# Kernel tuning notes

Measured on AMD Instinct MI355X. Metric: run time of the kernel, lower is better.

Reference implementation:

```python
import jax, jax.numpy as jnp
import numpy as np

B, T, D, H, W = 2, 16, 64, 64, 64
K = 3      # kernel_size
EXP = 2    # mlp expand
EPS = 1e-5


def _ln(x, w, b):
    mu = jnp.mean(x, axis=-1, keepdims=True)
    var = jnp.mean(jnp.square(x - mu), axis=-1, keepdims=True)
    return (x - mu) * jax.lax.rsqrt(var + EPS) * w + b


def _cnorm(z, w, b):
    zc = jnp.concatenate([z.real, z.imag], axis=-1)
    zn = _ln(zc, w, b)
    r, i = jnp.split(zn, 2, axis=-1)
    return jax.lax.complex(r, i)


def _conv(x, w):
    return jax.lax.conv_general_dilated(x, w, (1, 1), 'SAME',
                                        dimension_numbers=('NCHW', 'OIHW', 'NCHW'))


def setup_inputs() -> dict:
    key = jax.random.key(0)
    ks = jax.random.split(key, 16)
    def n(k, shp, s=0.02):
        return jax.random.normal(k, shp, jnp.float32) * s
    eye = jnp.eye(D, dtype=jnp.float32)
    return {
        'x_real': jax.random.normal(ks[0], (B, T, D, H, W), jnp.float32),
        'x_imag': jax.random.normal(ks[1], (B, T, D, H, W), jnp.float32),
        'dt': jax.random.uniform(ks[2], (B, T), jnp.float32, 0.5, 1.5),
        'ln_s_w': jnp.ones(2 * D, jnp.float32), 'ln_s_b': jnp.zeros(2 * D, jnp.float32),
        'ln_t_w': jnp.ones(2 * D, jnp.float32), 'ln_t_b': jnp.zeros(2 * D, jnp.float32),
        'ln_m_w': jnp.ones(2 * D, jnp.float32), 'ln_m_b': jnp.zeros(2 * D, jnp.float32),
        'cw_r': n(ks[3], (D, D, K, K)), 'cw_i': n(ks[4], (D, D, K, K)),
        'cb_r': jnp.zeros(D, jnp.float32), 'cb_i': jnp.zeros(D, jnp.float32),
        'spec_wr': 1.0 + n(ks[5], (D, H, W)), 'spec_wi': n(ks[6], (D, H, W)),
        'gate': jnp.full((1,), 0.5, jnp.float32),
        'lam_re': n(ks[7], (D,), 0.5), 'lam_im': n(ks[8], (D,), 0.5),
        'V_re': eye + n(ks[9], (D, D), 0.1), 'V_im': n(ks[10], (D, D), 0.1),
        'Vinv_re': eye + n(ks[11], (D, D), 0.1), 'Vinv_im': n(ks[12], (D, D), 0.1),
        'mlp_w1': n(ks[13], (2 * D, 2 * D * EXP)), 'mlp_b1': jnp.zeros(2 * D * EXP, jnp.float32),
        'mlp_w2': n(ks[14], (2 * D * EXP, 2 * D)), 'mlp_b2': jnp.zeros(2 * D, jnp.float32),
    }


def _forward(x_real, x_imag, dt, ln_s_w, ln_s_b, ln_t_w, ln_t_b, ln_m_w, ln_m_b,
             cw_r, cw_i, cb_r, cb_i, spec_wr, spec_wi, gate, lam_re, lam_im,
             V_re, V_im, Vinv_re, Vinv_im, mlp_w1, mlp_b1, mlp_w2, mlp_b2):
    x = jax.lax.complex(x_real, x_imag)          # (B,T,D,H,W) complex64
    # ---- spatial mixing: complex-norm -> gated blend of Clifford conv and spectral mix ----
    resid = x
    xs = x.reshape(B * T, D, H, W)
    xs = _cnorm(xs.transpose(0, 2, 3, 1), ln_s_w, ln_s_b).transpose(0, 3, 1, 2)
    xr, xi = xs.real, xs.imag
    o_r = _conv(xr, cw_r) - _conv(xi, cw_i) + cb_r[None, :, None, None]
    o_i = _conv(xr, cw_i) + _conv(xi, cw_r) + cb_i[None, :, None, None]
    cliff = jax.lax.complex(o_r, o_i)
    wspec = jax.lax.complex(spec_wr, spec_wi)    # (D,H,W) learned spectral multiplier
    spec = jnp.fft.ifft2(jnp.fft.fft2(xs, axes=(-2, -1)) * wspec[None], axes=(-2, -1))
    g = gate[0]
    x = (g * cliff + (1.0 - g) * spec).reshape(B, T, D, H, W) + resid
    # ---- temporal mixing: eigenbasis projection + diagonal parallel scan ----
    resid = x
    x_t = x.transpose(0, 3, 4, 1, 2).reshape(B * H * W, T, D)
    x_t = _cnorm(x_t, ln_t_w, ln_t_b)
    dt_exp = jnp.repeat(dt, H * W, axis=0)                         # (B*H*W, T)
    lam = jax.lax.complex(-jax.nn.softplus(lam_re), lam_im)        # (D,)
    evo = jnp.exp(lam[None, None, :] * dt_exp[:, :, None])         # (B*H*W, T, D)
    x_eig = x_t @ jax.lax.complex(Vinv_re, Vinv_im).T
    def comb(c1, c2):
        a1, b1 = c1
        a2, b2 = c2
        return (a1 * a2, a2 * b1 + b2)
    _, h = jax.lax.associative_scan(comb, (evo, x_eig), axis=1)    # h_t = a_t h_{t-1} + x_t, h_0 = 0
    xt_out = h @ jax.lax.complex(V_re, V_im).T
    x = xt_out.reshape(B, H, W, T, D).transpose(0, 3, 4, 1, 2) + resid
    # ---- complex MLP ----
    resid = x
    xc = x.transpose(0, 1, 3, 4, 2)                                 # (B,T,H,W,D)
    zc = _ln(jnp.concatenate([xc.real, xc.imag], axis=-1), ln_m_w, ln_m_b)
    hmid = jax.nn.gelu(zc @ mlp_w1 + mlp_b1, approximate=False)
    zo = hmid @ mlp_w2 + mlp_b2
    r, i = jnp.split(zo, 2, axis=-1)
    x = jax.lax.complex(r, i).transpose(0, 1, 4, 2, 3) + resid
    # complex output represented as real pair on trailing axis
    return jnp.stack([x.real, x.imag], axis=-1)                     # (B,T,D,H,W,2)


def reference(x_real, x_imag, dt, ln_s_w, ln_s_b, ln_t_w, ln_t_b, ln_m_w, ln_m_b,
              cw_r, cw_i, cb_r, cb_i, spec_wr, spec_wi, gate, lam_re, lam_im,
              V_re, V_im, Vinv_re, Vinv_im, mlp_w1, mlp_b1, mlp_w2, mlp_b2):
    return _forward(x_real, x_imag, dt, ln_s_w, ln_s_b, ln_t_w, ln_t_b, ln_m_w, ln_m_b,
                    cw_r, cw_i, cb_r, cb_i, spec_wr, spec_wi, gate, lam_re, lam_im,
                    V_re, V_im, Vinv_re, Vinv_im, mlp_w1, mlp_b1, mlp_w2, mlp_b2)
```

## Files before the change

kernel.cpp:

```cpp
#include <hip/hip_runtime.h>
#include <math.h>

#define NELEM 8388608
#define HW    4096
#define DCH   64
#define TT    16
#define EPS   1e-5f

typedef __attribute__((ext_vector_type(8))) short bfrag;
typedef __attribute__((ext_vector_type(16))) float accv;

__device__ __forceinline__ unsigned short f2b(float f) {
  union { float f; unsigned u; } v; v.f = f;
  unsigned r = (v.u + 0x7FFF + ((v.u >> 16) & 1)) >> 16;
  return (unsigned short)r;
}
__device__ __forceinline__ float b2f(unsigned short h) {
  union { unsigned u; float f; } v; v.u = ((unsigned)h) << 16;
  return v.f;
}
__device__ __forceinline__ int rev4(int x) {
  return ((x & 3) << 4) | (x & 12) | ((x >> 4) & 3);
}
__device__ __forceinline__ int xcd_swizzle(int bid, int nb) {
  return (bid & 7) * (nb >> 3) + (bid >> 3);
}

__device__ __forceinline__ float2 c_add(float2 a, float2 b) {
  return make_float2(a.x + b.x, a.y + b.y);
}
__device__ __forceinline__ float2 c_sub(float2 a, float2 b) {
  return make_float2(a.x - b.x, a.y - b.y);
}
__device__ __forceinline__ float2 c_mul_conj(float2 a, float2 w) {
  return make_float2(a.x * w.x + a.y * w.y, a.y * w.x - a.x * w.y);
}
__device__ __forceinline__ float2 c_mul_pos(float2 a, float2 w) {
  return make_float2(a.x * w.x - a.y * w.y, a.y * w.x + a.x * w.y);
}
__device__ __forceinline__ float2 shfl_xor2(float2 v, int m) {
  return make_float2(__shfl_xor(v.x, m), __shfl_xor(v.y, m));
}
__device__ __forceinline__ float gelu_f(float v) {
  float y = -1.595769122f * (v + 0.044715f * v * v * v);
  return v * __builtin_amdgcn_rcpf(1.f + __expf(y));
}

__global__ __launch_bounds__(256) void k_wprep(
    const float* __restrict__ cwr, const float* __restrict__ cwi,
    unsigned short* __restrict__ Wt) {
  int gid = blockIdx.x * 256 + threadIdx.x;
  if (gid >= 9 * 128 * 128) return;
  int j = gid & 7;
  int lane = (gid >> 3) & 63;
  int t2 = (gid >> 9) & 1;
  int cb = (gid >> 10) & 1;
  int ks = (gid >> 11) & 3;
  int half = (gid >> 13) & 1;
  int tap = gid >> 14;
  int l31 = lane & 31, lhi = lane >> 5;
  int co = cb * 64 + t2 * 32 + l31;
  int c = half * 64 + ks * 16 + lhi * 8 + j;
  int kh = tap / 3, kw = tap - kh * 3;
  int dout = co & 63, cin = c & 63;
  int widx = ((dout * 64 + cin) * 3 + kh) * 3 + kw;
  float v;
  if (co < 64) v = (c < 64) ? cwr[widx] : -cwi[widx];
  else         v = (c < 64) ? cwi[widx] :  cwr[widx];
  Wt[gid] = f2b(v);
}

__global__ __launch_bounds__(256) void k_vprep(
    const float* __restrict__ Vre, const float* __restrict__ Vim,
    const float* __restrict__ Vire, const float* __restrict__ Viim,
    unsigned short* __restrict__ Wt1, unsigned short* __restrict__ Wt2) {
  int gid = blockIdx.x * 256 + threadIdx.x;
  int j = gid & 7, n = (gid >> 3) & 127, kg = gid >> 10;
  int k = kg * 8 + j;
  int d = k & 63, dp = n & 63;
  float v1, v2;
  if (k < 64) {
    v1 = (n < 64) ? Vire[dp * 64 + d] : Viim[dp * 64 + d];
    v2 = (n < 64) ? Vre[dp * 64 + d] : Vim[dp * 64 + d];
  } else {
    v1 = (n < 64) ? -Viim[dp * 64 + d] : Vire[dp * 64 + d];
    v2 = (n < 64) ? -Vim[dp * 64 + d] : Vre[dp * 64 + d];
  }
  Wt1[gid] = f2b(v1); Wt2[gid] = f2b(v2);
}

__global__ __launch_bounds__(256) void k_mprep(
    const float* __restrict__ w1, const float* __restrict__ w2,
    unsigned short* __restrict__ Wm) {
  int gid = blockIdx.x * 256 + threadIdx.x;
  int j = gid & 7, n = (gid >> 3) & 127, kgh = (gid >> 10) & 31;
  int hh = kgh >> 4, kg = kgh & 15;
  float v;
  if (gid < 32768) v = w1[(kg * 8 + j) * 256 + hh * 128 + n];
  else             v = w2[(hh * 128 + kg * 8 + j) * 128 + n];
  Wm[gid] = f2b(v);
}

__global__ __launch_bounds__(256) void k_sprep(
    const float* __restrict__ swr, const float* __restrict__ swi,
    float2* __restrict__ Ps) {
  int gid = blockIdx.x * 256 + threadIdx.x;
  int cy = gid & 63, j = (gid >> 6) & 15, p = (gid >> 10) & 3, ch = gid >> 12;
  int kap = ((p & 1) << 1) | (p >> 1);
  int fr = ((j & 3) << 4) | (((j >> 2) & 3) << 2) | kap;
  int addr = ch * 4096 + fr * 64 + rev4(cy);
  Ps[gid] = make_float2(swr[addr], swi[addr]);
}

__global__ __launch_bounds__(256) void k_ln_spatial(
    const float* __restrict__ xr, const float* __restrict__ xi,
    const float* __restrict__ w, const float* __restrict__ b,
    unsigned short* __restrict__ Xb) {
  int gid = blockIdx.x * 256 + threadIdx.x;
  int bt = gid >> 12;
  int hw = gid & 4095;
  size_t base = (size_t)bt * DCH * HW + hw;
  float vr[DCH], vi[DCH];
  float s = 0.f, s2 = 0.f;
#pragma unroll
  for (int d = 0; d < DCH; ++d) {
    float a = xr[base + d * HW];
    float c = xi[base + d * HW];
    vr[d] = a; vi[d] = c;
    s += a + c;
    s2 += a * a + c * c;
  }
  float mu = s * (1.f / 128.f);
  float var = s2 * (1.f / 128.f) - mu * mu;
  float rs = rsqrtf(var + EPS);
  unsigned short* dst = Xb + ((size_t)gid << 7);
#pragma unroll
  for (int k = 0; k < 8; ++k) {
    int4 o;
    unsigned short* op = (unsigned short*)&o;
#pragma unroll
    for (int j = 0; j < 8; ++j) {
      int d = k * 8 + j;
      op[j] = f2b((vr[d] - mu) * rs * w[d] + b[d]);
    }
    ((int4*)dst)[k] = o;
  }
#pragma unroll
  for (int k = 0; k < 8; ++k) {
    int4 o;
    unsigned short* op = (unsigned short*)&o;
#pragma unroll
    for (int j = 0; j < 8; ++j) {
      int d = k * 8 + j;
      op[j] = f2b((vi[d] - mu) * rs * w[64 + d] + b[64 + d]);
    }
    ((int4*)(dst + 64))[k] = o;
  }
}

__global__ __launch_bounds__(256) void k_xpose(
    const unsigned short* __restrict__ Xb,
    unsigned short* __restrict__ Xc) {
  int bid = xcd_swizzle(blockIdx.x, 1024);
  int n = bid >> 5, chp = bid & 31;
  int tid = threadIdx.x;
  const unsigned short* src = Xb + (((size_t)n * 4096) << 7) + (chp << 1);
  size_t dst0 = (((size_t)n * 64 + chp * 2) << 13);
#pragma unroll
  for (int half = 0; half < 2; ++half) {
    union { unsigned short u[16]; int4 v[2]; } a0, a1;
#pragma unroll
    for (int m = 0; m < 16; ++m) {
      int hw = tid * 16 + m;
      unsigned vv = *(const unsigned*)(src + ((size_t)hw << 7) + (half << 6));
      a0.u[m] = (unsigned short)(vv & 0xffffu);
      a1.u[m] = (unsigned short)(vv >> 16);
    }
    *(int4*)(Xc + dst0 + (half << 12) + tid * 16)            = a0.v[0];
    *(int4*)(Xc + dst0 + (half << 12) + tid * 16 + 8)        = a0.v[1];
    *(int4*)(Xc + dst0 + 8192 + (half << 12) + tid * 16)     = a1.v[0];
    *(int4*)(Xc + dst0 + 8192 + (half << 12) + tid * 16 + 8) = a1.v[1];
  }
}

__global__ __launch_bounds__(256, 4) void k_conv_mfma(
    const unsigned short* __restrict__ Xb,
    const unsigned short* __restrict__ Wt,
    const float* __restrict__ br, const float* __restrict__ bi,
    unsigned short* __restrict__ Cb) {
  __shared__ unsigned short Xs[4 * 8 * 66 * 8];
  int bid = xcd_swizzle(blockIdx.x, 1024);
  int rg = bid & 31, n = bid >> 5;
  int r0 = rg << 1;
  int tid = threadIdx.x;
  int lane = tid & 63, wv = tid >> 6;
  int l31 = lane & 31, lhi = lane >> 5;
  int cb = wv >> 1;
  int cobase = cb << 6;
  int prow = wv & 1;

  accv acc[4] = {accv{}, accv{}, accv{}, accv{}};

  for (int q = tid; q < 2112; q += 256)
    ((int4*)Xs)[q] = make_int4(0, 0, 0, 0);
  __syncthreads();

  for (int half = 0; half < 2; ++half) {
    for (int q = tid; q < 2048; q += 256) {
      int cs = q & 7, col = (q >> 3) & 63, j = q >> 9;
      int gr = r0 - 1 + j;
      if (gr >= 0 && gr < 64) {
        const int4 v = *(const int4*)(Xb + (((size_t)n * 4096 + gr * 64 + col) << 7)
                                      + (half << 6) + (cs << 3));
        *(int4*)(Xs + (((j * 8 + cs) * 66 + col + 1) << 3)) = v;
      }
    }
    __syncthreads();
#pragma unroll
    for (int tap = 0; tap < 9; ++tap) {
      int kh = tap / 3, kw = tap - kh * 3;
#pragma unroll
      for (int ks = 0; ks < 4; ++ks) {
        bfrag af[2], bfv[2];
        const unsigned short* wf =
            Wt + ((((((tap * 2 + half) * 4 + ks) * 2 + cb) * 2) * 64) + lane) * 8;
        af[0] = *(const bfrag*)wf;
        af[1] = *(const bfrag*)(wf + 512);
        const unsigned short* xrow = Xs + ((((prow + kh) * 8 + (ks * 2 + lhi)) * 66 + kw) << 3);
#pragma unroll
        for (int u = 0; u < 2; ++u)
          bfv[u] = *(const bfrag*)(xrow + ((u * 32 + l31) << 3));
#pragma unroll
        for (int t2 = 0; t2 < 2; ++t2)
#pragma unroll
          for (int u = 0; u < 2; ++u)
            acc[t2 * 2 + u] = __builtin_amdgcn_mfma_f32_32x32x16_bf16(
                af[t2], bfv[u], acc[t2 * 2 + u], 0, 0, 0);
      }
    }
    __syncthreads();
  }

#pragma unroll
  for (int t2 = 0; t2 < 2; ++t2) {
#pragma unroll
    for (int u = 0; u < 2; ++u) {
      accv A = acc[t2 * 2 + u];
      int hw = (r0 + prow) * 64 + u * 32 + l31;
#pragma unroll
      for (int rr = 0; rr < 16; ++rr) {
        int co = cobase + t2 * 32 + (rr & 3) + ((rr >> 2) << 3) + (lhi << 2);
        float bias = (co < 64) ? br[co] : bi[co & 63];
        Cb[(((size_t)n * 128 + co) << 12) + hw] = f2b(A[rr] + bias);
      }
    }
  }
}

__global__ __launch_bounds__(256) void k_fft_blend(
    float* __restrict__ Xr, float* __restrict__ Xi,
    const unsigned short* __restrict__ Xc,
    const unsigned short* __restrict__ Cb,
    const float* __restrict__ rr_, const float* __restrict__ ri_,
    const float* __restrict__ swr, const float* __restrict__ swi,
    const float2* __restrict__ Ps,
    const float* __restrict__ gate) {
  __shared__ __align__(16) float2 sc[64 * 66];
  __shared__ float2 tw[64];
  int bid = xcd_swizzle(blockIdx.x, 2048);
  int ch = bid & 63;
  int n = bid >> 6;
  int base = bid << 12;
  int tid = threadIdx.x;
  int lane = tid & 63, wv = tid >> 6;
  int l15 = lane & 15;
  int p = lane >> 4;
  int kap = ((p & 1) << 1) | (p >> 1);
  bool pswap = (p & 1), prot = (p & 2);
  float sA = prot ? -1.f : 1.f;
  float sB = pswap ? -1.f : 1.f;
  int r = wv * 16 + l15;
  int cy = r;

  if (tid < 64) {
    float sv, cv;
    __sincosf(0.09817477042468103f * (float)tid, &sv, &cv);
    tw[tid] = make_float2(cv, sv);
  }

  float2 x[16];
  {
    const unsigned short* xp = Xc + ((size_t)bid << 13) + r * 64 + 16 * p;
    int4 ra = *(const int4*)xp;
    int4 rb = *(const int4*)(xp + 8);
    int4 ia = *(const int4*)(xp + 4096);
    int4 ib = *(const int4*)(xp + 4104);
    const unsigned short* rap = (const unsigned short*)&ra;
    const unsigned short* rbp = (const unsigned short*)&rb;
    const unsigned short* iap = (const unsigned short*)&ia;
    const unsigned short* ibp = (const unsigned short*)&ib;
#pragma unroll
    for (int j = 0; j < 8; ++j) {
      x[j]     = make_float2(b2f(rap[j]), b2f(iap[j]));
      x[8 + j] = make_float2(b2f(rbp[j]), b2f(ibp[j]));
    }
  }
  __syncthreads();

#pragma unroll
  for (int j = 0; j < 16; ++j) {
    float2 mine = x[j];
    float2 pr = shfl_xor2(mine, 32);
    float2 t = make_float2(pr.x + sA * mine.x, pr.y + sA * mine.y);
    float2 pr2 = shfl_xor2(t, 16);
    float2 low = pswap ? pr2 : t;
    float2 high = pswap ? t : pr2;
    float2 u = prot ? make_float2(high.y, -high.x) : high;
    float2 o = make_float2(low.x + sB * u.x, low.y + sB * u.y);
    x[j] = c_mul_conj(o, tw[kap * j]);
  }
#pragma unroll
  for (int b = 0; b < 4; ++b) {
    float2 t0 = c_add(x[b], x[b + 8]), t1 = c_sub(x[b], x[b + 8]);
    float2 t2 = c_add(x[b + 4], x[b + 12]), t3 = c_sub(x[b + 4], x[b + 12]);
    x[b] = c_add(t0, t2);
    float2 u1 = make_float2(t1.x + t3.y, t1.y - t3.x);
    float2 u2 = c_sub(t0, t2);
    float2 u3 = make_float2(t1.x - t3.y, t1.y + t3.x);
    x[b + 4] = c_mul_conj(u1, tw[4 * b]);
    x[b + 8] = c_mul_conj(u2, tw[8 * b]);
    x[b + 12] = c_mul_conj(u3, tw[12 * b]);
  }
#pragma unroll
  for (int a = 0; a < 4; ++a) {
    int a4 = 4 * a;
    float2 t0 = c_add(x[a4], x[a4 + 2]), t1 = c_sub(x[a4], x[a4 + 2]);
    float2 t2 = c_add(x[a4 + 1], x[a4 + 3]), t3 = c_sub(x[a4 + 1], x[a4 + 3]);
    x[a4] = c_add(t0, t2);
    x[a4 + 1] = make_float2(t1.x + t3.y, t1.y - t3.x);
    x[a4 + 2] = c_sub(t0, t2);
    x[a4 + 3] = make_float2(t1.x - t3.y, t1.y + t3.x);
  }
#pragma unroll
  for (int q = 0; q < 8; ++q) {
    float4 v = make_float4(x[2 * q].x, x[2 * q].y, x[2 * q + 1].x, x[2 * q + 1].y);
    *(float4*)&sc[r * 66 + 16 * kap + 2 * q] = v;
  }
  __syncthreads();

#pragma unroll
  for (int j = 0; j < 16; ++j)
    x[j] = sc[(16 * p + j) * 66 + cy];
#pragma unroll
  for (int j = 0; j < 16; ++j) {
    float2 mine = x[j];
    float2 pr = shfl_xor2(mine, 32);
    float2 t = make_float2(pr.x + sA * mine.x, pr.y + sA * mine.y);
    float2 pr2 = shfl_xor2(t, 16);
    float2 low = pswap ? pr2 : t;
    float2 high = pswap ? t : pr2;
    float2 u = prot ? make_float2(high.y, -high.x) : high;
    float2 o = make_float2(low.x + sB * u.x, low.y + sB * u.y);
    x[j] = c_mul_conj(o, tw[kap * j]);
  }
#pragma unroll
  for (int b = 0; b < 4; ++b) {
    float2 t0 = c_add(x[b], x[b + 8]), t1 = c_sub(x[b], x[b + 8]);
    float2 t2 = c_add(x[b + 4], x[b + 12]), t3 = c_sub(x[b + 4], x[b + 12]);
    x[b] = c_add(t0, t2);
    float2 u1 = make_float2(t1.x + t3.y, t1.y - t3.x);
    float2 u2 = c_sub(t0, t2);
    float2 u3 = make_float2(t1.x - t3.y, t1.y + t3.x);
    x[b + 4] = c_mul_conj(u1, tw[4 * b]);
    x[b + 8] = c_mul_conj(u2, tw[8 * b]);
    x[b + 12] = c_mul_conj(u3, tw[12 * b]);
  }
#pragma unroll
  for (int a = 0; a < 4; ++a) {
    int a4 = 4 * a;
    float2 t0 = c_add(x[a4], x[a4 + 2]), t1 = c_sub(x[a4], x[a4 + 2]);
    float2 t2 = c_add(x[a4 + 1], x[a4 + 3]), t3 = c_sub(x[a4 + 1], x[a4 + 3]);
    x[a4] = c_add(t0, t2);
    x[a4 + 1] = make_float2(t1.x + t3.y, t1.y - t3.x);
    x[a4 + 2] = c_sub(t0, t2);
    x[a4 + 3] = make_float2(t1.x - t3.y, t1.y + t3.x);
  }

  if (Ps) {
    const float2* pp = Ps + (((size_t)(ch * 4 + p) * 16) << 6) + r;
#pragma unroll
    for (int j = 0; j < 16; ++j) {
      float2 w = pp[j * 64];
      float2 v = x[j];
      x[j] = make_float2(v.x * w.x - v.y * w.y, v.x * w.y + v.y * w.x);
    }
  } else {
    int fb = ch * 4096 + rev4(cy);
#pragma unroll
    for (int j = 0; j < 16; ++j) {
      int fr = ((j & 3) << 4) | (((j >> 2) & 3) << 2) | kap;
      float wr = swr[fb + fr * 64];
      float wi = swi[fb + fr * 64];
      float2 v = x[j];
      x[j] = make_float2(v.x * wr - v.y * wi, v.x * wi + v.y * wr);
    }
  }

#pragma unroll
  for (int a = 0; a < 4; ++a) {
    int a4 = 4 * a;
    float2 e0 = c_add(x[a4], x[a4 + 2]), e1 = c_sub(x[a4], x[a4 + 2]);
    float2 o0 = c_add(x[a4 + 1], x[a4 + 3]), o1 = c_sub(x[a4 + 1], x[a4 + 3]);
    x[a4] = c_add(e0, o0);
    x[a4 + 1] = make_float2(e1.x - o1.y, e1.y + o1.x);
    x[a4 + 2] = c_sub(e0, o0);
    x[a4 + 3] = make_float2(e1.x + o1.y, e1.y - o1.x);
  }
#pragma unroll
  for (int b = 0; b < 4; ++b) {
    float2 v1 = c_mul_pos(x[b + 4], tw[4 * b]);
    float2 v2 = c_mul_pos(x[b + 8], tw[8 * b]);
    float2 v3 = c_mul_pos(x[b + 12], tw[12 * b]);
    float2 e0 = c_add(x[b], v2), e1 = c_sub(x[b], v2);
    float2 o0 = c_add(v1, v3), o1 = c_sub(v1, v3);
    x[b] = c_add(e0, o0);
    x[b + 4] = make_float2(e1.x - o1.y, e1.y + o1.x);
    x[b + 8] = c_sub(e0, o0);
    x[b + 12] = make_float2(e1.x + o1.y, e1.y - o1.x);
  }
#pragma unroll
  for (int j = 0; j < 16; ++j) {
    float2 mine = c_mul_pos(x[j], tw[kap * j]);
    float2 pr = shfl_xor2(mine, 16);
    float2 t = make_float2(pr.x + sB * mine.x, pr.y + sB * mine.y);
    float2 pr2 = shfl_xor2(t, 32);
    float2 low = prot ? pr2 : t;
    float2 high = prot ? t : pr2;
    float2 u = pswap ? make_float2(-high.y, high.x) : high;
    x[j] = make_float2(low.x + sA * u.x, low.y + sA * u.y);
  }
#pragma unroll
  for (int j = 0; j < 16; ++j)
    sc[(16 * p + j) * 66 + cy] = x[j];
  __syncthreads();

#pragma unroll
  for (int q = 0; q < 8; ++q) {
    float4 v = *(const float4*)&sc[r * 66 + 16 * p + 2 * q];
    x[2 * q] = make_float2(v.x, v.y);
    x[2 * q + 1] = make_float2(v.z, v.w);
  }
#pragma unroll
  for (int a = 0; a < 4; ++a) {
    int a4 = 4 * a;
    float2 e0 = c_add(x[a4], x[a4 + 2]), e1 = c_sub(x[a4], x[a4 + 2]);
    float2 o0 = c_add(x[a4 + 1], x[a4 + 3]), o1 = c_sub(x[a4 + 1], x[a4 + 3]);
    x[a4] = c_add(e0, o0);
    x[a4 + 1] = make_float2(e1.x - o1.y, e1.y + o1.x);
    x[a4 + 2] = c_sub(e0, o0);
    x[a4 + 3] = make_float2(e1.x + o1.y, e1.y - o1.x);
  }
#pragma unroll
  for (int b = 0; b < 4; ++b) {
    float2 v1 = c_mul_pos(x[b + 4], tw[4 * b]);
    float2 v2 = c_mul_pos(x[b + 8], tw[8 * b]);
    float2 v3 = c_mul_pos(x[b + 12], tw[12 * b]);
    float2 e0 = c_add(x[b], v2), e1 = c_sub(x[b], v2);
    float2 o0 = c_add(v1, v3), o1 = c_sub(v1, v3);
    x[b] = c_add(e0, o0);
    x[b + 4] = make_float2(e1.x - o1.y, e1.y + o1.x);
    x[b + 8] = c_sub(e0, o0);
    x[b + 12] = make_float2(e1.x + o1.y, e1.y - o1.x);
  }
#pragma unroll
  for (int j = 0; j < 16; ++j) {
    float2 mine = c_mul_pos(x[j], tw[p * j]);
    float2 pr = shfl_xor2(mine, 32);
    float2 t = make_float2(pr.x + sA * mine.x, pr.y + sA * mine.y);
    float2 pr2 = shfl_xor2(t, 16);
    float2 low = pswap ? pr2 : t;
    float2 high = pswap ? t : pr2;
    float2 u = prot ? make_float2(-high.y, high.x) : high;
    x[j] = make_float2(low.x + sB * u.x, low.y + sB * u.y);
  }
  __syncthreads();

#pragma unroll
  for (int q = 0; q < 8; ++q) {
    float4 v = make_float4(x[2 * q].x, x[2 * q].y, x[2 * q + 1].x, x[2 * q + 1].y);
    *(float4*)&sc[r * 66 + 16 * kap + 2 * q] = v;
  }
  __syncthreads();

  float g = gate[0];
  const float scale = 1.f / 4096.f;
  for (int idx = tid; idx < 4096; idx += 256) {
    int rr2 = idx >> 6, cc2 = idx & 63;
    float2 sp = sc[rr2 * 66 + cc2];
    int a = base + idx;
    float cr = b2f(Cb[(((size_t)n * 128 + ch) << 12) + idx]);
    float ci = b2f(Cb[(((size_t)n * 128 + 64 + ch) << 12) + idx]);
    Xr[a] = g * cr + (1.f - g) * sp.x * scale + rr_[a];
    Xi[a] = g * ci + (1.f - g) * sp.y * scale + ri_[a];
  }
}

__global__ __launch_bounds__(256, 3) void k_temporal_mfma(
    float* __restrict__ Xr, float* __restrict__ Xi,
    const float* __restrict__ dt,
    const float* __restrict__ lnw, const float* __restrict__ lnb,
    const float* __restrict__ lam_re, const float* __restrict__ lam_im,
    const unsigned short* __restrict__ Wt1, const unsigned short* __restrict__ Wt2) {
  __shared__ unsigned short Asub[16 * 64 * 8];
  __shared__ float Xe[64 * 129];
  int bid = xcd_swizzle(blockIdx.x, 2048);
  int b = bid >> 10, tile = bid & 1023;
  int hw0 = tile * 4;
  int tid = threadIdx.x;
  int lane = tid & 63, wv = tid >> 6;
  int l31 = lane & 31, lhi = lane >> 5;
  size_t xbase = (size_t)b * TT * DCH * HW + hw0;

  float4 res[8];
#pragma unroll
  for (int q = 0; q < 8; ++q) {
    int item = tid + q * 256;
    int t = item >> 7, c = item & 127;
    int d = c & 63;
    const float* src = ((c >> 6) ? Xi : Xr) + xbase + ((size_t)t * 64 + d) * HW;
    float4 v = *(const float4*)src;
    res[q] = v;
    Xe[(t * 4 + 0) * 129 + c] = v.x;
    Xe[(t * 4 + 1) * 129 + c] = v.y;
    Xe[(t * 4 + 2) * 129 + c] = v.z;
    Xe[(t * 4 + 3) * 129 + c] = v.w;
  }
  __syncthreads();

  {
    int row = tid >> 2, seg = tid & 3;
    float s = 0.f, s2 = 0.f;
#pragma unroll
    for (int j = 0; j < 32; ++j) {
      float v = Xe[row * 129 + seg * 32 + j];
      s += v; s2 += v * v;
    }
    s += __shfl_xor(s, 1); s2 += __shfl_xor(s2, 1);
    s += __shfl_xor(s, 2); s2 += __shfl_xor(s2, 2);
    float mu = s * (1.f / 128.f);
    float var = s2 * (1.f / 128.f) - mu * mu;
    float rs = rsqrtf(var + EPS);
#pragma unroll
    for (int k = 0; k < 16; ++k) {
      int c = k * 8 + seg * 2;
      float v0 = (Xe[row * 129 + c] - mu) * rs * lnw[c] + lnb[c];
      float v1 = (Xe[row * 129 + c + 1] - mu) * rs * lnw[c + 1] + lnb[c + 1];
      unsigned pk = (unsigned)f2b(v0) | ((unsigned)f2b(v1) << 16);
      *(unsigned*)(Asub + (k * 64 + row) * 8 + seg * 2) = pk;
    }
  }
  __syncthreads();

  int mt = wv & 1, ntb = (wv >> 1) << 1;
  accv acc0 = accv{}, acc1 = accv{};
#pragma unroll
  for (int ks = 0; ks < 8; ++ks) {
    int kg = ks * 2 + lhi;
    bfrag a = *(const bfrag*)(Asub + (kg * 64 + mt * 32 + l31) * 8);
    bfrag b0 = *(const bfrag*)(Wt1 + (kg * 128 + ntb * 32 + l31) * 8);
    bfrag b1 = *(const bfrag*)(Wt1 + (kg * 128 + (ntb + 1) * 32 + l31) * 8);
    acc0 = __builtin_amdgcn_mfma_f32_32x32x16_bf16(a, b0, acc0, 0, 0, 0);
    acc1 = __builtin_amdgcn_mfma_f32_32x32x16_bf16(a, b1, acc1, 0, 0, 0);
  }
  __syncthreads();

#pragma unroll
  for (int rr = 0; rr < 16; ++rr) {
    int mrow = mt * 32 + (rr & 3) + ((rr >> 2) << 3) + (lhi << 2);
    Xe[mrow * 129 + ntb * 32 + l31] = acc0[rr];
    Xe[mrow * 129 + (ntb + 1) * 32 + l31] = acc1[rr];
  }
  __syncthreads();

  {
    int px = tid & 3, dp = tid >> 2;
    float x0 = lam_re[dp];
    float nl = -(x0 > 15.f ? x0 : log1pf(__expf(x0)));
    float li = lam_im[dp];
    float hr = 0.f, hi = 0.f;
    int cR = dp, cI = 64 + dp;
    for (int t = 0; t < TT; ++t) {
      float dtv = dt[b * 16 + t];
      float ea = __expf(nl * dtv);
      float sv, cv; __sincosf(li * dtv, &sv, &cv);
      float evr = ea * cv, evi = ea * sv;
      int r = t * 4 + px;
      float xr_ = Xe[r * 129 + cR], xi_ = Xe[r * 129 + cI];
      float nhr = evr * hr - evi * hi + xr_;
      float nhi = evr * hi + evi * hr + xi_;
      hr = nhr; hi = nhi;
      Asub[((cR >> 3) * 64 + r) * 8 + (cR & 7)] = f2b(hr);
      Asub[((cI >> 3) * 64 + r) * 8 + (cI & 7)] = f2b(hi);
    }
  }
  __syncthreads();

  acc0 = accv{}; acc1 = accv{};
#pragma unroll
  for (int ks = 0; ks < 8; ++ks) {
    int kg = ks * 2 + lhi;
    bfrag a = *(const bfrag*)(Asub + (kg * 64 + mt * 32 + l31) * 8);
    bfrag b0 = *(const bfrag*)(Wt2 + (kg * 128 + ntb * 32 + l31) * 8);
    bfrag b1 = *(const bfrag*)(Wt2 + (kg * 128 + (ntb + 1) * 32 + l31) * 8);
    acc0 = __builtin_amdgcn_mfma_f32_32x32x16_bf16(a, b0, acc0, 0, 0, 0);
    acc1 = __builtin_amdgcn_mfma_f32_32x32x16_bf16(a, b1, acc1, 0, 0, 0);
  }
  __syncthreads();

#pragma unroll
  for (int rr = 0; rr < 16; ++rr) {
    int mrow = mt * 32 + (rr & 3) + ((rr >> 2) << 3) + (lhi << 2);
    Xe[mrow * 129 + ntb * 32 + l31] = acc0[rr];
    Xe[mrow * 129 + (ntb + 1) * 32 + l31] = acc1[rr];
  }
  __syncthreads();

#pragma unroll
  for (int q = 0; q < 8; ++q) {
    int item = tid + q * 256;
    int t = item >> 7, c = item & 127;
    int d = c & 63;
    float* dst = ((c >> 6) ? Xi : Xr) + xbase + ((size_t)t * 64 + d) * HW;
    float4 o;
    o.x = Xe[(t * 4 + 0) * 129 + c] + res[q].x;
    o.y = Xe[(t * 4 + 1) * 129 + c] + res[q].y;
    o.z = Xe[(t * 4 + 2) * 129 + c] + res[q].z;
    o.w = Xe[(t * 4 + 3) * 129 + c] + res[q].w;
    *(float4*)dst = o;
  }
}

__global__ __launch_bounds__(256, 4) void k_mlp_pre(
    const float* __restrict__ Xr, const float* __restrict__ Xi,
    const float* __restrict__ lnw, const float* __restrict__ lnb,
    const unsigned short* __restrict__ Wm1,
    const unsigned short* __restrict__ Wm2,
    const float* __restrict__ b1, const float* __restrict__ b2,
    float* __restrict__ out) {
  __shared__ __align__(16) unsigned char smem[32768];
  float* Xe = (float*)smem;
  unsigned short* Asub = (unsigned short*)smem;
  unsigned short* mid  = (unsigned short*)(smem + 16384);
  unsigned short* ost  = (unsigned short*)smem;
  int bid = blockIdx.x;
  int bt = bid >> 6, tile = bid & 63;
  int hw0 = tile << 6;
  int tid = threadIdx.x;
  int lane = tid & 63, wv = tid >> 6;
  int l31 = lane & 31, lhi = lane >> 5;
  size_t base = (size_t)bt * DCH * HW + hw0;

#pragma unroll
  for (int q = 0; q < 8; ++q) {
    int item = q * 256 + tid;
    int m4 = item & 15, c = item >> 4;
    int d = c & 63;
    const float* src = ((c >> 6) ? Xi : Xr) + base + (size_t)d * HW + m4 * 4;
    *(float4*)(Xe + c * 64 + m4 * 4) = *(const float4*)src;
  }
  __syncthreads();

  {
    int row = tid >> 2, seg = tid & 3;
    float xv[32];
    float s = 0.f, s2 = 0.f;
#pragma unroll
    for (int j = 0; j < 32; ++j) {
      float v = Xe[(seg * 32 + j) * 64 + row];
      xv[j] = v; s += v; s2 += v * v;
    }
    s += __shfl_xor(s, 1); s2 += __shfl_xor(s2, 1);
    s += __shfl_xor(s, 2); s2 += __shfl_xor(s2, 2);
    float mu = s * (1.f / 128.f);
    float var = s2 * (1.f / 128.f) - mu * mu;
    float rs = rsqrtf(var + EPS);
    __syncthreads();
#pragma unroll
    for (int j = 0; j < 32; ++j) {
      int c = seg * 32 + j;
      Asub[((c >> 3) * 64 + row) * 8 + (c & 7)] =
          f2b((xv[j] - mu) * rs * lnw[c] + lnb[c]);
    }
  }
  __syncthreads();

  int ng = wv * 32 + l31;
  accv c0 = accv{}, c1 = accv{};
#pragma unroll
  for (int h = 0; h < 2; ++h) {
    accv g0 = accv{}, g1 = accv{};
#pragma unroll
    for (int ks = 0; ks < 8; ++ks) {
      int kg = ks * 2 + lhi;
      bfrag bfr = *(const bfrag*)(Wm1 + (((h * 16 + kg) * 128) + ng) * 8);
      bfrag a0 = *(const bfrag*)(Asub + (kg * 64 + l31) * 8);
      bfrag a1 = *(const bfrag*)(Asub + (kg * 64 + 32 + l31) * 8);
      g0 = __builtin_amdgcn_mfma_f32_32x32x16_bf16(a0, bfr, g0, 0, 0, 0);
      g1 = __builtin_amdgcn_mfma_f32_32x32x16_bf16(a1, bfr, g1, 0, 0, 0);
    }
    if (h == 1) __syncthreads();
    float b1v = b1[h * 128 + ng];
    int kgl = ng >> 3, jj = ng & 7;
#pragma unroll
    for (int rr = 0; rr < 16; ++rr) {
      int mr = (rr & 3) + ((rr >> 2) << 3) + (lhi << 2);
      mid[(kgl * 64 + mr) * 8 + jj] = f2b(gelu_f(g0[rr] + b1v));
      mid[(kgl * 64 + 32 + mr) * 8 + jj] = f2b(gelu_f(g1[rr] + b1v));
    }
    __syncthreads();
#pragma unroll
    for (int ks = 0; ks < 8; ++ks) {
      int kg = ks * 2 + lhi;
      bfrag bfr = *(const bfrag*)(Wm2 + (((h * 16 + kg) * 128) + ng) * 8);
      bfrag a0 = *(const bfrag*)(mid + (kg * 64 + l31) * 8);
      bfrag a1 = *(const bfrag*)(mid + (kg * 64 + 32 + l31) * 8);
      c0 = __builtin_amdgcn_mfma_f32_32x32x16_bf16(a0, bfr, c0, 0, 0, 0);
      c1 = __builtin_amdgcn_mfma_f32_32x32x16_bf16(a1, bfr, c1, 0, 0, 0);
    }
  }
  __syncthreads();

  {
    float b2v = b2[ng];
#pragma unroll
    for (int rr = 0; rr < 16; ++rr) {
      int mr = (rr & 3) + ((rr >> 2) << 3) + (lhi << 2);
      ost[ng * 66 + mr] = f2b(c0[rr] + b2v);
      ost[ng * 66 + 32 + mr] = f2b(c1[rr] + b2v);
    }
  }
  __syncthreads();
#pragma unroll
  for (int q = 0; q < 4; ++q) {
    int item = q * 256 + tid;
    int m4 = item & 15, d = item >> 4;
    size_t xa = base + (size_t)d * HW + m4 * 4;
    float4 xr4 = *(const float4*)(Xr + xa);
    float4 xi4 = *(const float4*)(Xi + xa);
    int m = m4 * 4;
    float r0 = b2f(ost[d * 66 + m]),     i0 = b2f(ost[(64 + d) * 66 + m]);
    float r1 = b2f(ost[d * 66 + m + 1]), i1 = b2f(ost[(64 + d) * 66 + m + 1]);
    float r2 = b2f(ost[d * 66 + m + 2]), i2 = b2f(ost[(64 + d) * 66 + m + 2]);
    float r3 = b2f(ost[d * 66 + m + 3]), i3 = b2f(ost[(64 + d) * 66 + m + 3]);
    float4 o1, o2;
    o1.x = r0 + xr4.x; o1.y = i0 + xi4.x; o1.z = r1 + xr4.y; o1.w = i1 + xi4.y;
    o2.x = r2 + xr4.z; o2.y = i2 + xi4.z; o2.z = r3 + xr4.w; o2.w = i3 + xi4.w;
    *(float4*)(out + xa * 2) = o1;
    *(float4*)(out + xa * 2 + 4) = o2;
  }
}

extern "C" void kernel_launch(void* const* d_in, const int* in_sizes, int n_in,
                              void* d_out, int out_size, void* d_ws, size_t ws_size,
                              hipStream_t stream) {
  const float* x_real  = (const float*)d_in[0];
  const float* x_imag  = (const float*)d_in[1];
  const float* dt      = (const float*)d_in[2];
  const float* ln_s_w  = (const float*)d_in[3];
  const float* ln_s_b  = (const float*)d_in[4];
  const float* ln_t_w  = (const float*)d_in[5];
  const float* ln_t_b  = (const float*)d_in[6];
  const float* ln_m_w  = (const float*)d_in[7];
  const float* ln_m_b  = (const float*)d_in[8];
  const float* cw_r    = (const float*)d_in[9];
  const float* cw_i    = (const float*)d_in[10];
  const float* cb_r    = (const float*)d_in[11];
  const float* cb_i    = (const float*)d_in[12];
  const float* spec_wr = (const float*)d_in[13];
  const float* spec_wi = (const float*)d_in[14];
  const float* gate    = (const float*)d_in[15];
  const float* lam_re  = (const float*)d_in[16];
  const float* lam_im  = (const float*)d_in[17];
  const float* V_re    = (const float*)d_in[18];
  const float* V_im    = (const float*)d_in[19];
  const float* Vinv_re = (const float*)d_in[20];
  const float* Vinv_im = (const float*)d_in[21];
  const float* mlp_w1  = (const float*)d_in[22];
  const float* mlp_b1  = (const float*)d_in[23];
  const float* mlp_w2  = (const float*)d_in[24];
  const float* mlp_b2  = (const float*)d_in[25];

  float* out = (float*)d_out;
  unsigned short* Xb = (unsigned short*)d_out;
  unsigned short* Cb = Xb + (size_t)2 * NELEM;
  unsigned short* Wt1 = Xb;
  unsigned short* Wt2 = Xb + 16384;
  float* W0r = (float*)d_ws;
  float* W0i = W0r + NELEM;
  unsigned short* Wt = (unsigned short*)d_ws;
  unsigned short* Xc = (unsigned short*)W0i;
  size_t ws_used = (size_t)2 * NELEM * 4;
  unsigned short* Wm = (unsigned short*)((char*)d_ws + ws_used);
  size_t ps_off = ws_used + 131072;
  bool sprep = ws_size >= ps_off + (size_t)262144 * 8;
  float2* Ps = sprep ? (float2*)((char*)d_ws + ps_off) : (float2*)nullptr;

  k_wprep<<<576, 256, 0, stream>>>(cw_r, cw_i, Wt);
  k_mprep<<<256, 256, 0, stream>>>(mlp_w1, mlp_w2, Wm);
  if (sprep) k_sprep<<<1024, 256, 0, stream>>>(spec_wr, spec_wi, Ps);
  k_ln_spatial<<<512, 256, 0, stream>>>(x_real, x_imag, ln_s_w, ln_s_b, Xb);
  k_xpose<<<1024, 256, 0, stream>>>(Xb, Xc);
  k_conv_mfma<<<1024, 256, 0, stream>>>(Xb, Wt, cb_r, cb_i, Cb);
  k_fft_blend<<<2048, 256, 0, stream>>>(W0r, W0i, Xc, Cb, x_real, x_imag,
                                        spec_wr, spec_wi, Ps, gate);
  k_vprep<<<64, 256, 0, stream>>>(V_re, V_im, Vinv_re, Vinv_im, Wt1, Wt2);
  k_temporal_mfma<<<2048, 256, 0, stream>>>(W0r, W0i, dt, ln_t_w, ln_t_b,
                                            lam_re, lam_im, Wt1, Wt2);
  k_mlp_pre<<<2048, 256, 0, stream>>>(W0r, W0i, ln_m_w, ln_m_b,
                                      Wm, Wm + 32768, mlp_b1, mlp_b2, out);
}
```

Baseline: 467.0 us.

## Stage spatial LayerNorm through LDS tiles for coalesced loads and stores

The spatial LayerNorm kernel now gives each block a 64-pixel tile. Each thread block loads all 128 channel rows as float4 into shared memory, and four threads cooperate on each pixel, combining their partial sums with lane shuffles. Normalized bf16 values are written back through shared memory so each pixel's 256-byte row goes out as int4 stores. This replaces the old one-thread-per-pixel design, which held 128 values in registers and wrote wide per-thread stores, in exchange for about 34 KB of LDS per block and extra barriers.

```diff
diff --git a/kernel.cpp b/kernel.cpp
--- a/kernel.cpp
+++ b/kernel.cpp
@@ -116,45 +116,60 @@
     const float* __restrict__ xr, const float* __restrict__ xi,
     const float* __restrict__ w, const float* __restrict__ b,
     unsigned short* __restrict__ Xb) {
-  int gid = blockIdx.x * 256 + threadIdx.x;
-  int bt = gid >> 12;
-  int hw = gid & 4095;
-  size_t base = (size_t)bt * DCH * HW + hw;
-  float vr[DCH], vi[DCH];
-  float s = 0.f, s2 = 0.f;
-#pragma unroll
-  for (int d = 0; d < DCH; ++d) {
-    float a = xr[base + d * HW];
-    float c = xi[base + d * HW];
-    vr[d] = a; vi[d] = c;
-    s += a + c;
-    s2 += a * a + c * c;
-  }
-  float mu = s * (1.f / 128.f);
-  float var = s2 * (1.f / 128.f) - mu * mu;
-  float rs = rsqrtf(var + EPS);
-  unsigned short* dst = Xb + ((size_t)gid << 7);
-#pragma unroll
-  for (int k = 0; k < 8; ++k) {
-    int4 o;
-    unsigned short* op = (unsigned short*)&o;
-#pragma unroll
-    for (int j = 0; j < 8; ++j) {
-      int d = k * 8 + j;
-      op[j] = f2b((vr[d] - mu) * rs * w[d] + b[d]);
-    }
-    ((int4*)dst)[k] = o;
-  }
-#pragma unroll
-  for (int k = 0; k < 8; ++k) {
-    int4 o;
-    unsigned short* op = (unsigned short*)&o;
-#pragma unroll
-    for (int j = 0; j < 8; ++j) {
-      int d = k * 8 + j;
-      op[j] = f2b((vi[d] - mu) * rs * w[64 + d] + b[64 + d]);
-    }
-    ((int4*)(dst + 64))[k] = o;
+  __shared__ __align__(16) unsigned char smem[34816];
+  float* Xe = (float*)smem;
+  unsigned short* ost = (unsigned short*)smem;
+  int bid = xcd_swizzle(blockIdx.x, 2048);
+  int bt = bid >> 6, tile = bid & 63;
+  int hw0 = tile << 6;
+  int tid = threadIdx.x;
+  size_t base = (size_t)bt * DCH * HW + hw0;
+
+#pragma unroll
+  for (int q = 0; q < 8; ++q) {
+    int item = q * 256 + tid;
+    int m4 = item & 15, c = item >> 4;
+    int d = c & 63;
+    const float* src = ((c >> 6) ? xi : xr) + base + (size_t)d * HW + m4 * 4;
+    *(float4*)(Xe + c * 68 + m4 * 4) = *(const float4*)src;
+  }
+  __syncthreads();
+
+  {
+    int row = tid >> 2, seg = tid & 3;
+    float xv[32];
+    float s = 0.f, s2 = 0.f;
+#pragma unroll
+    for (int k = 0; k < 16; ++k) {
+      int c = k * 8 + seg * 2;
+      float v0 = Xe[c * 68 + row];
+      float v1 = Xe[(c + 1) * 68 + row];
+      xv[2 * k] = v0; xv[2 * k + 1] = v1;
+      s += v0 + v1; s2 += v0 * v0 + v1 * v1;
+    }
+    s += __shfl_xor(s, 1); s2 += __shfl_xor(s2, 1);
+    s += __shfl_xor(s, 2); s2 += __shfl_xor(s2, 2);
+    float mu = s * (1.f / 128.f);
+    float var = s2 * (1.f / 128.f) - mu * mu;
+    float rs = rsqrtf(var + EPS);
+    __syncthreads();
+#pragma unroll
+    for (int k = 0; k < 16; ++k) {
+      int c = k * 8 + seg * 2;
+      float v0 = (xv[2 * k] - mu) * rs * w[c] + b[c];
+      float v1 = (xv[2 * k + 1] - mu) * rs * w[c + 1] + b[c + 1];
+      unsigned pk = (unsigned)f2b(v0) | ((unsigned)f2b(v1) << 16);
+      *(unsigned*)(ost + row * 136 + c) = pk;
+    }
+  }
+  __syncthreads();
+
+#pragma unroll
+  for (int q = 0; q < 4; ++q) {
+    int item = q * 256 + tid;
+    int cq = item & 15, pix = item >> 4;
+    int4 v = *(const int4*)(ost + pix * 136 + cq * 8);
+    *(int4*)(Xb + (((size_t)bt * 4096 + hw0 + pix) << 7) + cq * 8) = v;
   }
 }
 
@@ -808,7 +823,7 @@
   k_wprep<<<576, 256, 0, stream>>>(cw_r, cw_i, Wt);
   k_mprep<<<256, 256, 0, stream>>>(mlp_w1, mlp_w2, Wm);
   if (sprep) k_sprep<<<1024, 256, 0, stream>>>(spec_wr, spec_wi, Ps);
-  k_ln_spatial<<<512, 256, 0, stream>>>(x_real, x_imag, ln_s_w, ln_s_b, Xb);
+  k_ln_spatial<<<2048, 256, 0, stream>>>(x_real, x_imag, ln_s_w, ln_s_b, Xb);
   k_xpose<<<1024, 256, 0, stream>>>(Xb, Xc);
   k_conv_mfma<<<1024, 256, 0, stream>>>(Xb, Wt, cb_r, cb_i, Cb);
   k_fft_blend<<<2048, 256, 0, stream>>>(W0r, W0i, Xc, Cb, x_real, x_imag,
```

Measured after the change: 435.6 us. 6.7% less time.
